# Kernel optimization log

Hardware: AMD Instinct MI355X
Metric: run time of the kernel (lower is better)

Reference implementation:

```python
import jax, jax.numpy as jnp
import numpy as np

D_MODEL, D_STATE, D_CONV, EXPAND, MLP_EXPAND = 1024, 16, 4, 2, 2
D_INNER = EXPAND * D_MODEL          # 2048
DT_RANK = D_MODEL // 16             # 64
B, L = 2, 1024


def setup_inputs() -> dict:
    key = jax.random.key(0)
    ks = jax.random.split(key, 16)
    s = 0.02
    inp = {
        "x": jax.random.normal(ks[0], (B, L, D_MODEL), jnp.float32),
        "ln1_w": jnp.ones((D_MODEL,), jnp.float32),
        "ln1_b": jnp.zeros((D_MODEL,), jnp.float32),
        "in_proj_w": jax.random.normal(ks[1], (2 * D_INNER, D_MODEL), jnp.float32) * s,
        "conv_w": jax.random.normal(ks[2], (D_INNER, 1, D_CONV), jnp.float32) * s,
        "conv_b": jnp.zeros((D_INNER,), jnp.float32),
        "x_proj_w": jax.random.normal(ks[3], (DT_RANK + 2 * D_STATE, D_INNER), jnp.float32) * s,
        "dt_proj_w": jax.random.normal(ks[4], (D_INNER, DT_RANK), jnp.float32) * s,
        "dt_proj_b": jax.random.uniform(ks[5], (D_INNER,), jnp.float32, -4.0, -2.0),
        "A_log": jnp.tile(jnp.log(jnp.arange(1, D_STATE + 1, dtype=jnp.float32))[None, :], (D_INNER, 1)),
        "D": jnp.ones((D_INNER,), jnp.float32),
        "out_proj_w": jax.random.normal(ks[6], (D_MODEL, D_INNER), jnp.float32) * s,
        "ln2_w": jnp.ones((D_MODEL,), jnp.float32),
        "ln2_b": jnp.zeros((D_MODEL,), jnp.float32),
        "mlp_w1": jax.random.normal(ks[7], (MLP_EXPAND * D_MODEL, D_MODEL), jnp.float32) * s,
        "mlp_b1": jnp.zeros((MLP_EXPAND * D_MODEL,), jnp.float32),
        "mlp_w2": jax.random.normal(ks[8], (D_MODEL, MLP_EXPAND * D_MODEL), jnp.float32) * s,
        "mlp_b2": jnp.zeros((D_MODEL,), jnp.float32),
    }
    return inp


def _layernorm(x, w, b, eps=1e-5):
    mu = jnp.mean(x, -1, keepdims=True)
    var = jnp.var(x, -1, keepdims=True)
    return (x - mu) * jax.lax.rsqrt(var + eps) * w + b


def _mamba(x, in_proj_w, conv_w, conv_b, x_proj_w, dt_proj_w, dt_proj_b, A_log, D, out_proj_w):
    # x: (B, L, d_model)
    xz = jnp.einsum('bld,ed->ble', x, in_proj_w)          # (B, L, 2*d_inner)
    u, z = jnp.split(xz, 2, axis=-1)                      # each (B, L, d_inner)
    # depthwise causal conv over time
    u_c = jnp.transpose(u, (0, 2, 1))                     # (B, d_inner, L)
    u_c = jax.lax.conv_general_dilated(
        u_c, conv_w, window_strides=(1,), padding=[(D_CONV - 1, 0)],
        dimension_numbers=('NCH', 'OIH', 'NCH'), feature_group_count=D_INNER)
    u = jax.nn.silu(jnp.transpose(u_c, (0, 2, 1)) + conv_b)  # (B, L, d_inner)

    dbc = jnp.einsum('bld,ed->ble', u, x_proj_w)          # (B, L, dt_rank+2*d_state)
    dt, Bm, Cm = jnp.split(dbc, [DT_RANK, DT_RANK + D_STATE], axis=-1)
    delta = jax.nn.softplus(jnp.einsum('blr,dr->bld', dt, dt_proj_w) + dt_proj_b)  # (B, L, d_inner)

    A = -jnp.exp(A_log)                                   # (d_inner, d_state)
    deltaA = jnp.exp(delta[..., None] * A)                # (B, L, d_inner, d_state)
    deltaBu = delta[..., None] * Bm[:, :, None, :] * u[..., None]

    def step(h, inp):
        dA, dBu, Ct = inp
        h = dA * h + dBu                                  # (B, d_inner, d_state)
        y = jnp.einsum('bdn,bn->bd', h, Ct)
        return h, y

    h0 = jnp.zeros((x.shape[0], D_INNER, D_STATE), x.dtype)
    xs = (jnp.moveaxis(deltaA, 1, 0), jnp.moveaxis(deltaBu, 1, 0), jnp.moveaxis(Cm, 1, 0))
    _, ys = jax.lax.scan(step, h0, xs)                    # (L, B, d_inner)
    y = jnp.moveaxis(ys, 0, 1) + u * D                    # (B, L, d_inner)
    y = y * jax.nn.silu(z)
    return jnp.einsum('ble,de->bld', y, out_proj_w)


def reference(x, ln1_w, ln1_b, in_proj_w, conv_w, conv_b, x_proj_w, dt_proj_w, dt_proj_b,
              A_log, D, out_proj_w, ln2_w, ln2_b, mlp_w1, mlp_b1, mlp_w2, mlp_b2):
    h = x + _mamba(_layernorm(x, ln1_w, ln1_b), in_proj_w, conv_w, conv_b,
                   x_proj_w, dt_proj_w, dt_proj_b, A_log, D, out_proj_w)
    y = _layernorm(h, ln2_w, ln2_b)
    y = jax.nn.gelu(jnp.einsum('bld,ed->ble', y, mlp_w1) + mlp_b1, approximate=False)
    y = jnp.einsum('ble,de->bld', y, mlp_w2) + mlp_b2
    return h + y
```

## Files before the change

kernel.cpp:

```cpp
#include <hip/hip_runtime.h>
#include <hip/hip_bf16.h>
#include <math.h>

typedef __hip_bfloat16 bf16;
typedef __attribute__((ext_vector_type(8))) short bf16x8;
typedef __attribute__((ext_vector_type(4))) float f32x4;

__device__ __forceinline__ float b2f(bf16 x) { return __bfloat162float(x); }
__device__ __forceinline__ float us2f(unsigned short u) {
    return __uint_as_float(((unsigned int)u) << 16);
}
__device__ __forceinline__ unsigned short f2us(float f) {
    bf16 t = __float2bfloat16(f);
    return *reinterpret_cast<unsigned short*>(&t);
}
__device__ __forceinline__ float scrub(float v) {
    return (v == v && fabsf(v) < 3.0e38f) ? v : 0.f;
}
__device__ __forceinline__ float to_float(float x) { return x; }
__device__ __forceinline__ float to_float(bf16 x) { return __bfloat162float(x); }
__device__ __forceinline__ void store_out(float* p, float v) { *p = v; }
__device__ __forceinline__ void store_out(bf16* p, float v) { *p = __float2bfloat16(v); }

__device__ __forceinline__ void ld8(const bf16* p, float* f) {
    const ushort4 a = ((const ushort4*)p)[0];
    const ushort4 b = ((const ushort4*)p)[1];
    f[0]=us2f(a.x); f[1]=us2f(a.y); f[2]=us2f(a.z); f[3]=us2f(a.w);
    f[4]=us2f(b.x); f[5]=us2f(b.y); f[6]=us2f(b.z); f[7]=us2f(b.w);
}

__device__ __forceinline__ void cp16(const void* g, void* l) {
    __builtin_amdgcn_global_load_lds(
        (const __attribute__((address_space(1))) unsigned int*)g,
        (__attribute__((address_space(3))) unsigned int*)l, 16, 0, 0);
}

struct Ptrs { const void* p[18]; };

__constant__ __device__ const long TOFF[19] = {
    0,         2097152,  2098176,  2099200,  6293504,  6301696,  6303744,
    6500352,   6631424,  6633472,  6666240,  6668288,  8765440,  8766464,
    8767488,   10864640, 10866688, 12963840, 12964864};

__global__ __launch_bounds__(256) void convert_kernel(
    Ptrs ptrs, unsigned short* __restrict__ dst)
{
    const long g = (long)blockIdx.x * 256 + threadIdx.x;
    if (g >= 1620608) return;
    const long e0 = g * 8;
    int t = 0;
    #pragma unroll
    for (int i = 1; i < 18; ++i) t += (e0 >= TOFF[i]) ? 1 : 0;
    const long local = e0 - TOFF[t];
    const float4* ps = (const float4*)((const float*)ptrs.p[t] + local);
    const float4 a = ps[0], b = ps[1];
    ushort4 o0, o1;
    o0.x = f2us(a.x); o0.y = f2us(a.y); o0.z = f2us(a.z); o0.w = f2us(a.w);
    o1.x = f2us(b.x); o1.y = f2us(b.y); o1.z = f2us(b.z); o1.w = f2us(b.w);
    *(ushort4*)(dst + e0)     = o0;
    *(ushort4*)(dst + e0 + 4) = o1;
}

template <typename TIN>
__global__ __launch_bounds__(256) void ln_kernel(
    const TIN* __restrict__ in, const bf16* __restrict__ gw,
    const bf16* __restrict__ gb, bf16* __restrict__ out)
{
    const int row = blockIdx.x;
    const int tid = threadIdx.x;
    float v[4];
    if constexpr (sizeof(TIN) == 2) {
        ushort4 raw = ((const ushort4*)((const unsigned short*)in + (long)row * 1024))[tid];
        v[0] = us2f(raw.x); v[1] = us2f(raw.y); v[2] = us2f(raw.z); v[3] = us2f(raw.w);
    } else {
        float4 raw = ((const float4*)((const float*)in + (long)row * 1024))[tid];
        v[0] = raw.x; v[1] = raw.y; v[2] = raw.z; v[3] = raw.w;
    }
    float s  = v[0] + v[1] + v[2] + v[3];
    float s2 = v[0]*v[0] + v[1]*v[1] + v[2]*v[2] + v[3]*v[3];
    #pragma unroll
    for (int o = 32; o > 0; o >>= 1) {
        s  += __shfl_xor(s, o);
        s2 += __shfl_xor(s2, o);
    }
    __shared__ float red[8];
    if ((tid & 63) == 0) { red[tid >> 6] = s; red[4 + (tid >> 6)] = s2; }
    __syncthreads();
    s  = red[0] + red[1] + red[2] + red[3];
    s2 = red[4] + red[5] + red[6] + red[7];
    const float mu  = s * (1.f / 1024.f);
    const float var = fmaxf(s2 * (1.f / 1024.f) - mu * mu, 0.f);
    const float rs  = rsqrtf(var + 1e-5f);
    const int c0 = tid * 4;
    ushort4 o;
    o.x = f2us((v[0] - mu) * rs * b2f(gw[c0 + 0]) + b2f(gb[c0 + 0]));
    o.y = f2us((v[1] - mu) * rs * b2f(gw[c0 + 1]) + b2f(gb[c0 + 1]));
    o.z = f2us((v[2] - mu) * rs * b2f(gw[c0 + 2]) + b2f(gb[c0 + 2]));
    o.w = f2us((v[3] - mu) * rs * b2f(gw[c0 + 3]) + b2f(gb[c0 + 3]));
    ((ushort4*)((unsigned short*)out + (long)row * 1024))[tid] = o;
}

template <int BM, int BN, int ACT, bool NG, int SK, typename TOUT, typename TRES>
__global__ __launch_bounds__(256) void gemm_as(
    const bf16* __restrict__ A, int lda,
    const bf16* __restrict__ Bw, int ldb,
    TOUT* __restrict__ C, int ldc,
    const bf16* __restrict__ bias,
    const TRES* __restrict__ res,
    int M, int N, int K)
{
    constexpr int AI = BM / 32;
    constexpr int BJ = BN / 32;
    __shared__ __align__(16) short As[BM * 64];
    __shared__ __align__(16) short Bs[BN * 64];
    const int tid  = threadIdx.x;
    const int lane = tid & 63;
    const int wv   = tid >> 6;
    const int m0 = blockIdx.y * BM;
    const int n0 = blockIdx.x * BN;
    if (SK > 1) {
        const int bz = blockIdx.z;
        A  += (long)bz * K;
        Bw += (long)bz * K;
        C  += (long)bz * M * (long)ldc;
    }
    const int wm = (wv >> 1) * (BM / 2);
    const int wn = (wv & 1) * (BN / 2);
    const int lr = lane & 15;
    const int lq = lane >> 4;
    const int grow = lane >> 3;
    const int gcol = (lane & 7) * 8;

    if (NG) {
        const int z0 = (N - n0) * 64;
        uint4 z; z.x = z.y = z.z = z.w = 0;
        for (int s = z0 + tid * 8; s < BN * 64; s += 2048)
            *(uint4*)&Bs[s] = z;
    }

    f32x4 acc[AI][BJ] = {};

    for (int k0 = 0; k0 < K; k0 += 64) {
        #pragma unroll
        for (int g = 0; g < BM / 32; ++g) {
            const int gg = g * 4 + wv;
            cp16(A + (long)(m0 + gg * 8 + grow) * lda + k0 + gcol, &As[gg * 512]);
        }
        #pragma unroll
        for (int g = 0; g < BN / 32; ++g) {
            const int gg = g * 4 + wv;
            if (!NG || n0 + gg * 8 < N)
                cp16(Bw + (long)(n0 + gg * 8 + grow) * ldb + k0 + gcol, &Bs[gg * 512]);
        }
        __syncthreads();

        #pragma unroll
        for (int kk = 0; kk < 2; ++kk) {
            bf16x8 af[AI], bfr[BJ];
            #pragma unroll
            for (int i = 0; i < AI; ++i)
                af[i] = *(const bf16x8*)&As[(wm + i * 16 + lr) * 64 + kk * 32 + lq * 8];
            #pragma unroll
            for (int j = 0; j < BJ; ++j)
                bfr[j] = *(const bf16x8*)&Bs[(wn + j * 16 + lr) * 64 + kk * 32 + lq * 8];
            #pragma unroll
            for (int i = 0; i < AI; ++i)
                #pragma unroll
                for (int j = 0; j < BJ; ++j)
                    acc[i][j] = __builtin_amdgcn_mfma_f32_16x16x32_bf16(
                        af[i], bfr[j], acc[i][j], 0, 0, 0);
        }
        __syncthreads();
    }

    #pragma unroll
    for (int j = 0; j < BJ; ++j) {
        const int col = n0 + wn + j * 16 + lr;
        if (col >= N) continue;
        const float bv = bias ? b2f(bias[col]) : 0.f;
        #pragma unroll
        for (int i = 0; i < AI; ++i) {
            const int r0 = m0 + wm + i * 16 + lq * 4;
            #pragma unroll
            for (int r = 0; r < 4; ++r) {
                const long row = r0 + r;
                float v = acc[i][j][r] + bv;
                if (ACT == 1) v = 0.5f * v * (1.f + erff(v * 0.70710678118f));
                if (ACT == 2) v = (v > 20.f) ? v : log1pf(__expf(v));
                if (res) v += to_float(res[row * (long)ldc + col]);
                store_out(&C[row * (long)ldc + col], scrub(v));
            }
        }
    }
}

__global__ __launch_bounds__(256) void splitk_reduce_kernel(
    const float* __restrict__ part, bf16* __restrict__ out)
{
    const int i = blockIdx.x * 256 + threadIdx.x;
    if (i >= 196608) return;
    float s = 0.f;
    #pragma unroll
    for (int z = 0; z < 8; ++z) s += part[(long)z * 196608 + i];
    out[i] = __float2bfloat16(s);
}

__global__ __launch_bounds__(256) void conv_silu_kernel(
    const bf16* __restrict__ xz, const bf16* __restrict__ cw,
    const bf16* __restrict__ cb, bf16* __restrict__ ucz)
{
    const int gid = blockIdx.x * 256 + threadIdx.x;
    const int row = gid >> 8;
    const int t   = row & 1023;
    const int d   = (gid & 255) * 8;

    float w[32];
    ld8(cw + d * 4,      w);
    ld8(cw + d * 4 + 8,  w + 8);
    ld8(cw + d * 4 + 16, w + 16);
    ld8(cw + d * 4 + 24, w + 24);

    float acc[8];
    ld8(cb + d, acc);
    #pragma unroll
    for (int j = 0; j < 4; ++j) {
        const int tt = t - 3 + j;
        if (tt >= 0) {
            float u[8];
            ld8(xz + (long)(row - 3 + j) * 4096 + d, u);
            #pragma unroll
            for (int k = 0; k < 8; ++k) acc[k] += w[k * 4 + j] * u[k];
        }
    }
    ushort4 o0, o1;
    unsigned short* po = (unsigned short*)&o0;
    #pragma unroll
    for (int k = 0; k < 8; ++k) {
        const float v = acc[k] / (1.f + __expf(-acc[k]));
        ((unsigned short*)&o0)[k & 3 | ((k >> 2) << 31)] = 0;
        if (k < 4) ((unsigned short*)&o0)[k] = f2us(v);
        else       ((unsigned short*)&o1)[k - 4] = f2us(v);
    }
    (void)po;
    ((ushort4*)(ucz + (long)row * 4096 + d))[0] = o0;
    ((ushort4*)(ucz + (long)row * 4096 + d))[1] = o1;

    float z8[8];
    ld8(xz + (long)row * 4096 + 2048 + d, z8);
    #pragma unroll
    for (int k = 0; k < 8; ++k) {
        const float v = z8[k] / (1.f + __expf(-z8[k]));
        if (k < 4) ((unsigned short*)&o0)[k] = f2us(v);
        else       ((unsigned short*)&o1)[k - 4] = f2us(v);
    }
    ((ushort4*)(ucz + (long)row * 4096 + 2048 + d))[0] = o0;
    ((ushort4*)(ucz + (long)row * 4096 + 2048 + d))[1] = o1;
}

__device__ __forceinline__ int swizzle_d0(int bx) {
    return ((bx & 7) << 8) | ((bx >> 3) << 4);
}

__global__ __launch_bounds__(256) void scan_local_kernel(
    const bf16* __restrict__ delta,
    const bf16* __restrict__ ucz,
    const bf16* __restrict__ dbc,
    const float* __restrict__ A_log,
    const float* __restrict__ Dp,
    bf16* __restrict__ y_local,
    bf16* __restrict__ Pbuf,
    bf16* __restrict__ H)
{
    const int d0  = swizzle_d0(blockIdx.x);
    const int b   = blockIdx.y;
    const int sg  = blockIdx.z;
    const int tid = threadIdx.x;
    const int n   = tid & 15;
    const int dl  = tid >> 4;
    const int d   = d0 + dl;

    __shared__ float2         sDU[32][16];
    __shared__ float2         sBC[32][16];
    __shared__ float          sZ [32][16];
    __shared__ unsigned short sPc[32][16];
    __shared__ unsigned short sY [32][16];
    __shared__ float          sP [16 * 336];

    const float An = -expf(A_log[d * 16 + n]);
    const float Dd = Dp[d];
    const long rowbase = (long)b * 1024 + sg * 32;

    const int wv  = tid >> 6;
    const int pdl = 4 * wv + ((tid & 63) >> 4);
    const int ptq = tid & 15;

    #pragma unroll
    for (int k = 0; k < 2; ++k) {
        const int i  = k * 256 + tid;
        const int tt = i >> 4, dd = i & 15;
        const long r = rowbase + tt;
        sDU[tt][dd] = float2{b2f(delta[r * 2048 + d0 + dd]),
                             b2f(ucz  [r * 4096 + d0 + dd])};
        sZ[tt][dd]  = b2f(ucz[r * 4096 + 2048 + d0 + dd]);
    }
    #pragma unroll
    for (int k = 0; k < 4; ++k) {
        const int i  = k * 256 + tid;
        const int tt = i >> 5, c = i & 31;
        ((float*)&sBC[tt][0])[(c & 15) * 2 + (c >> 4)] =
            b2f(dbc[(rowbase + tt) * 96 + 64 + c]);
    }
    __syncthreads();

    float h = 0.f, Pc = 0.f;
    #pragma unroll
    for (int half = 0; half < 2; ++half) {
        #pragma unroll 4
        for (int tl = 0; tl < 16; ++tl) {
            const int t = half * 16 + tl;
            const float2 du = sDU[t][dl];
            const float2 bc = sBC[t][n];
            Pc += du.x;
            const float a = __expf(du.x * An);
            h = a * h + (du.x * du.y) * bc.x;
            float p = h * bc.y;
            if (n == 0) { p += du.y * Dd; sPc[t][dl] = f2us(Pc); }
            sP[dl * 336 + tl * 20 + n] = p;
        }
        {
            const int t = half * 16 + ptq;
            const float4* pp = (const float4*)&sP[pdl * 336 + ptq * 20];
            const float4 p0 = pp[0], p1 = pp[1], p2 = pp[2], p3 = pp[3];
            const float s = ((p0.x + p0.y) + (p0.z + p0.w))
                          + ((p1.x + p1.y) + (p1.z + p1.w))
                          + ((p2.x + p2.y) + (p2.z + p2.w))
                          + ((p3.x + p3.y) + (p3.z + p3.w));
            sY[t][pdl] = f2us(s * sZ[t][pdl]);
        }
    }
    __syncthreads();

    #pragma unroll
    for (int k = 0; k < 2; ++k) {
        const int i  = k * 256 + tid;
        const int tt = i >> 4, dd = i & 15;
        const long r = rowbase + tt;
        ((unsigned short*)y_local)[r * 2048 + d0 + dd] = sY[tt][dd];
        ((unsigned short*)Pbuf)  [r * 2048 + d0 + dd] = sPc[tt][dd];
    }

    H[((long)(b * 32 + sg) * 2048 + d) * 16 + n] = __float2bfloat16(h);
}

__global__ __launch_bounds__(256) void scan_combine_kernel(
    const bf16*  __restrict__ Pbuf,
    const float* __restrict__ A_log,
    bf16* __restrict__ H)
{
    const int gid = blockIdx.x * 256 + threadIdx.x;
    const int b  = gid >> 15;
    const int dn = gid & 32767;
    const int d  = dn >> 4;
    const float An = -expf(A_log[dn]);
    float hin = 0.f;
    for (int s = 0; s < 32; ++s) {
        const long idx = (long)(b * 32 + s) * 32768 + dn;
        const float hout = b2f(H[idx]);
        H[idx] = __float2bfloat16(hin);
        const float Pend = b2f(Pbuf[((long)b * 1024 + s * 32 + 31) * 2048 + d]);
        hin = hout + __expf(An * Pend) * hin;
    }
}

__global__ __launch_bounds__(256) void scan_fix_kernel(
    bf16* __restrict__ y,
    const bf16* __restrict__ Pbuf,
    const bf16* __restrict__ dbc,
    const bf16* __restrict__ ucz,
    const float* __restrict__ A_log,
    const bf16* __restrict__ H)
{
    const int d0  = swizzle_d0(blockIdx.x);
    const int b   = blockIdx.y;
    const int sg  = blockIdx.z;
    const int tid = threadIdx.x;
    const long rowb = (long)b * 1024 + sg * 32;

    __shared__ float sH [16][16];
    __shared__ float sAn[16][16];
    __shared__ float sCc[32][16];

    sH [tid >> 4][tid & 15] = b2f(H[(long)(b * 32 + sg) * 32768 + d0 * 16 + tid]);
    sAn[tid >> 4][tid & 15] = -expf(A_log[d0 * 16 + tid]);
    for (int i = tid; i < 512; i += 256)
        sCc[i >> 4][i & 15] = b2f(dbc[(rowb + (i >> 4)) * 96 + 80 + (i & 15)]);
    __syncthreads();

    const int dd = tid & 15;
    float4 An4[4], H4[4];
    #pragma unroll
    for (int j = 0; j < 4; ++j) {
        An4[j] = *(const float4*)&sAn[dd][j * 4];
        H4[j]  = *(const float4*)&sH [dd][j * 4];
    }

    #pragma unroll
    for (int k = 0; k < 2; ++k) {
        const int t = k * 16 + (tid >> 4);
        const long row = rowb + t;
        const float P = us2f(((const unsigned short*)Pbuf)[row * 2048 + d0 + dd]);
        float corr = 0.f;
        #pragma unroll
        for (int j = 0; j < 4; ++j) {
            const float4 C4 = *(const float4*)&sCc[t][j * 4];
            corr += C4.x * __expf(An4[j].x * P) * H4[j].x;
            corr += C4.y * __expf(An4[j].y * P) * H4[j].y;
            corr += C4.z * __expf(An4[j].z * P) * H4[j].z;
            corr += C4.w * __expf(An4[j].w * P) * H4[j].w;
        }
        const float slz = b2f(ucz[row * 4096 + 2048 + d0 + dd]);
        const float yl  = b2f(y[row * 2048 + d0 + dd]);
        y[row * 2048 + d0 + dd] = __float2bfloat16(yl + slz * corr);
    }
}

extern "C" void kernel_launch(void* const* d_in, const int* in_sizes, int n_in,
                              void* d_out, int out_size, void* d_ws, size_t ws_size,
                              hipStream_t stream)
{
    char* ws = (char*)d_ws;
    const size_t MiB = 1048576;
    const size_t HMiB = 524288;

    bf16*  ucz  = (bf16*)(ws);
    bf16*  dbc  = (bf16*)(ws + 16 * MiB);
    bf16*  xn   = (bf16*)(ws + 16 * MiB + HMiB);
    bf16*  dlb  = (bf16*)(ws + 16 * MiB + HMiB);
    bf16*  xz   = (bf16*)(ws + 20 * MiB + HMiB);
    float* xpart= (float*)(ws + 20 * MiB + HMiB);
    bf16*  Pbuf = (bf16*)(ws + 24 * MiB + HMiB);
    bf16*  Hbuf = (bf16*)(ws + 32 * MiB + HMiB);
    float* hb   = (float*)(ws);
    bf16*  hn   = (bf16*)(ws +  8 * MiB);
    bf16*  gb   = (bf16*)(ws + 24 * MiB + HMiB);
    unsigned short* cvt = (unsigned short*)(ws + 37 * MiB);

    const float* xf     = (const float*)d_in[0];
    const float* A_logf = (const float*)d_in[9];
    const float* Dpf    = (const float*)d_in[10];

    const bf16* ln1_w      = (const bf16*)(cvt + 2097152);
    const bf16* ln1_b      = (const bf16*)(cvt + 2098176);
    const bf16* in_proj_w  = (const bf16*)(cvt + 2099200);
    const bf16* conv_w     = (const bf16*)(cvt + 6293504);
    const bf16* conv_b     = (const bf16*)(cvt + 6301696);
    const bf16* x_proj_w   = (const bf16*)(cvt + 6303744);
    const bf16* dt_proj_w  = (const bf16*)(cvt + 6500352);
    const bf16* dt_proj_b  = (const bf16*)(cvt + 6631424);
    const bf16* out_proj_w = (const bf16*)(cvt + 6668288);
    const bf16* ln2_w      = (const bf16*)(cvt + 8765440);
    const bf16* ln2_b      = (const bf16*)(cvt + 8766464);
    const bf16* mlp_w1     = (const bf16*)(cvt + 8767488);
    const bf16* mlp_b1     = (const bf16*)(cvt + 10864640);
    const bf16* mlp_w2     = (const bf16*)(cvt + 10866688);
    const bf16* mlp_b2     = (const bf16*)(cvt + 12963840);

    Ptrs ptrs;
    for (int i = 0; i < 18; ++i) ptrs.p[i] = d_in[i];
    convert_kernel<<<6332, 256, 0, stream>>>(ptrs, cvt);

    ln_kernel<float><<<2048, 256, 0, stream>>>(xf, ln1_w, ln1_b, xn);
    gemm_as<128, 128, 0, false, 1, bf16, bf16><<<dim3(32, 16), 256, 0, stream>>>(
        xn, 1024, in_proj_w, 1024, xz, 4096, nullptr, (const bf16*)nullptr, 2048, 4096, 1024);
    conv_silu_kernel<<<2048, 256, 0, stream>>>(xz, conv_w, conv_b, ucz);
    gemm_as<64, 64, 0, true, 8, float, bf16><<<dim3(2, 32, 8), 256, 0, stream>>>(
        ucz, 4096, x_proj_w, 2048, xpart, 96, nullptr, (const bf16*)nullptr, 2048, 96, 256);
    splitk_reduce_kernel<<<768, 256, 0, stream>>>(xpart, dbc);
    gemm_as<128, 64, 2, false, 1, bf16, bf16><<<dim3(32, 16), 256, 0, stream>>>(
        dbc, 96, dt_proj_w, 64, dlb, 2048, dt_proj_b, (const bf16*)nullptr, 2048, 2048, 64);
    scan_local_kernel<<<dim3(128, 2, 32), 256, 0, stream>>>(
        dlb, ucz, dbc, A_logf, Dpf, dlb, Pbuf, Hbuf);
    scan_combine_kernel<<<256, 256, 0, stream>>>(Pbuf, A_logf, Hbuf);
    scan_fix_kernel<<<dim3(128, 2, 32), 256, 0, stream>>>(
        dlb, Pbuf, dbc, ucz, A_logf, Hbuf);
    gemm_as<64, 64, 0, false, 1, float, float><<<dim3(16, 32), 256, 0, stream>>>(
        dlb, 2048, out_proj_w, 2048, hb, 1024, nullptr, xf, 2048, 1024, 2048);
    ln_kernel<float><<<2048, 256, 0, stream>>>(hb, ln2_w, ln2_b, hn);
    gemm_as<128, 64, 1, false, 1, bf16, bf16><<<dim3(32, 16), 256, 0, stream>>>(
        hn, 1024, mlp_w1, 1024, gb, 2048, mlp_b1, (const bf16*)nullptr, 2048, 2048, 1024);
    gemm_as<64, 64, 0, false, 1, float, float><<<dim3(16, 32), 256, 0, stream>>>(
        gb, 2048, mlp_w2, 2048, (float*)d_out, 1024, mlp_b2, hb, 2048, 1024, 2048);
}
```

Before: 364.1 us.

## Use shuffle reduction in scan_local and prefetch loads in scan_combine

scan_local now reduces the per-state products across the 16 lanes with xor shuffles instead of staging them in a large shared buffer, which removes that buffer and one pass through it. It also adds an occupancy hint to the launch bounds. scan_combine now loads all 32 segment states and decay factors into registers before the serial recurrence, so the loop no longer waits on dependent global loads. The leftover dead stores in the conv kernel are removed. The cost is more register pressure and more shuffle instructions.

```diff
diff --git a/kernel.cpp b/kernel.cpp
--- a/kernel.cpp
+++ b/kernel.cpp
@@ -233,15 +233,12 @@
         }
     }
     ushort4 o0, o1;
-    unsigned short* po = (unsigned short*)&o0;
     #pragma unroll
     for (int k = 0; k < 8; ++k) {
         const float v = acc[k] / (1.f + __expf(-acc[k]));
-        ((unsigned short*)&o0)[k & 3 | ((k >> 2) << 31)] = 0;
-        if (k < 4) ((unsigned short*)&o0)[k] = f2us(v);
+        if (k < 4) ((unsigned short*)&o0)[k]     = f2us(v);
         else       ((unsigned short*)&o1)[k - 4] = f2us(v);
     }
-    (void)po;
     ((ushort4*)(ucz + (long)row * 4096 + d))[0] = o0;
     ((ushort4*)(ucz + (long)row * 4096 + d))[1] = o1;
 
@@ -250,7 +247,7 @@
     #pragma unroll
     for (int k = 0; k < 8; ++k) {
         const float v = z8[k] / (1.f + __expf(-z8[k]));
-        if (k < 4) ((unsigned short*)&o0)[k] = f2us(v);
+        if (k < 4) ((unsigned short*)&o0)[k]     = f2us(v);
         else       ((unsigned short*)&o1)[k - 4] = f2us(v);
     }
     ((ushort4*)(ucz + (long)row * 4096 + 2048 + d))[0] = o0;
@@ -261,7 +258,7 @@
     return ((bx & 7) << 8) | ((bx >> 3) << 4);
 }
 
-__global__ __launch_bounds__(256) void scan_local_kernel(
+__global__ __launch_bounds__(256, 6) void scan_local_kernel(
     const bf16* __restrict__ delta,
     const bf16* __restrict__ ucz,
     const bf16* __restrict__ dbc,
@@ -284,15 +281,10 @@
     __shared__ float          sZ [32][16];
     __shared__ unsigned short sPc[32][16];
     __shared__ unsigned short sY [32][16];
-    __shared__ float          sP [16 * 336];
 
     const float An = -expf(A_log[d * 16 + n]);
     const float Dd = Dp[d];
     const long rowbase = (long)b * 1024 + sg * 32;
-
-    const int wv  = tid >> 6;
-    const int pdl = 4 * wv + ((tid & 63) >> 4);
-    const int ptq = tid & 15;
 
     #pragma unroll
     for (int k = 0; k < 2; ++k) {
@@ -314,28 +306,30 @@
 
     float h = 0.f, Pc = 0.f;
     #pragma unroll
-    for (int half = 0; half < 2; ++half) {
-        #pragma unroll 4
-        for (int tl = 0; tl < 16; ++tl) {
-            const int t = half * 16 + tl;
+    for (int q = 0; q < 4; ++q) {
+        float p[8];
+        #pragma unroll
+        for (int tl = 0; tl < 8; ++tl) {
+            const int t = q * 8 + tl;
             const float2 du = sDU[t][dl];
             const float2 bc = sBC[t][n];
             Pc += du.x;
             const float a = __expf(du.x * An);
             h = a * h + (du.x * du.y) * bc.x;
-            float p = h * bc.y;
-            if (n == 0) { p += du.y * Dd; sPc[t][dl] = f2us(Pc); }
-            sP[dl * 336 + tl * 20 + n] = p;
-        }
-        {
-            const int t = half * 16 + ptq;
-            const float4* pp = (const float4*)&sP[pdl * 336 + ptq * 20];
-            const float4 p0 = pp[0], p1 = pp[1], p2 = pp[2], p3 = pp[3];
-            const float s = ((p0.x + p0.y) + (p0.z + p0.w))
-                          + ((p1.x + p1.y) + (p1.z + p1.w))
-                          + ((p2.x + p2.y) + (p2.z + p2.w))
-                          + ((p3.x + p3.y) + (p3.z + p3.w));
-            sY[t][pdl] = f2us(s * sZ[t][pdl]);
+            p[tl] = h * bc.y;
+            if (n == 0) { p[tl] += du.y * Dd; sPc[t][dl] = f2us(Pc); }
+        }
+        #pragma unroll
+        for (int tl = 0; tl < 8; ++tl) {
+            float r = p[tl];
+            r += __shfl_xor(r, 1);
+            r += __shfl_xor(r, 2);
+            r += __shfl_xor(r, 4);
+            r += __shfl_xor(r, 8);
+            if (n == 0) {
+                const int t = q * 8 + tl;
+                sY[t][dl] = f2us(r * sZ[t][dl]);
+            }
         }
     }
     __syncthreads();
@@ -362,13 +356,20 @@
     const int dn = gid & 32767;
     const int d  = dn >> 4;
     const float An = -expf(A_log[dn]);
+
+    float Hh[32], E[32];
+    #pragma unroll
+    for (int s = 0; s < 32; ++s)
+        Hh[s] = b2f(H[(long)(b * 32 + s) * 32768 + dn]);
+    #pragma unroll
+    for (int s = 0; s < 32; ++s)
+        E[s] = __expf(An * b2f(Pbuf[((long)b * 1024 + s * 32 + 31) * 2048 + d]));
+
     float hin = 0.f;
+    #pragma unroll
     for (int s = 0; s < 32; ++s) {
-        const long idx = (long)(b * 32 + s) * 32768 + dn;
-        const float hout = b2f(H[idx]);
-        H[idx] = __float2bfloat16(hin);
-        const float Pend = b2f(Pbuf[((long)b * 1024 + s * 32 + 31) * 2048 + d]);
-        hin = hout + __expf(An * Pend) * hin;
+        H[(long)(b * 32 + s) * 32768 + dn] = __float2bfloat16(hin);
+        hin = Hh[s] + E[s] * hin;
     }
 }
 
```

Result: slower. 401.3 us (+10.2%).
